# Performance work log

Hardware: AMD Instinct MI355X
Metric: run time of the kernel (lower is better)

The kernel has to match this reference:

```python
import jax, jax.numpy as jnp
import numpy as np

HEADS = 8
DIM_HEAD = 64
DIM = 512
SCALE = DIM ** -0.5  # NOTE: original scales by dim**-0.5, not dim_head**-0.5


def setup_inputs() -> dict:
    key = jax.random.key(0)
    k1, k2, k3 = jax.random.split(key, 3)
    b, n = 2, 4096
    x = jax.random.normal(k1, (b, n, DIM), dtype=jnp.float32)
    Wqkv = jax.random.normal(k2, (DIM, 3 * HEADS * DIM_HEAD), dtype=jnp.float32) * (DIM ** -0.5)
    Wout = jax.random.normal(k3, (HEADS * DIM_HEAD, DIM), dtype=jnp.float32) * ((HEADS * DIM_HEAD) ** -0.5)
    b_out = jnp.zeros((DIM,), dtype=jnp.float32)
    return {"x": x, "Wqkv": Wqkv, "Wout": Wout, "b_out": b_out}


def reference(x, Wqkv, Wout, b_out):
    b, n, _ = x.shape
    h, d = HEADS, DIM_HEAD
    qkv = x @ Wqkv  # [b, n, 3*h*d]
    q, k, v = jnp.split(qkv, 3, axis=-1)
    to_heads = lambda t: t.reshape(b, n, h, d).transpose(0, 2, 1, 3)  # [b,h,n,d]
    q, k, v = to_heads(q), to_heads(k), to_heads(v)
    half = n // 2
    q_s, q_t = q[:, :, :half], q[:, :, half:]
    k_t = k[:, :, half:]  # k_s is unused in the original module
    v_s, v_t = v[:, :, :half], v[:, :, half:]
    # temporal branch: q_t attends to k_t, reads v_t
    dots_t = jnp.einsum('bhid,bhjd->bhij', q_t, k_t) * SCALE
    # spatial branch: cross-term q_s attends to k_t, reads v_s
    dots_s = jnp.einsum('bhid,bhjd->bhij', q_s, k_t) * SCALE
    attn_s = jax.nn.softmax(dots_s, axis=-1)
    attn_t = jax.nn.softmax(dots_t, axis=-1)
    out_s = jnp.einsum('bhij,bhjd->bhid', attn_s, v_s)
    out_t = jnp.einsum('bhij,bhjd->bhid', attn_t, v_t)
    out = jnp.concatenate([out_s, out_t], axis=2)  # [b,h,n,d]
    out = out.transpose(0, 2, 1, 3).reshape(b, n, h * d)
    return out @ Wout + b_out
```

## Files before the change

### kernel.cpp

```cpp
#include <hip/hip_runtime.h>
#include <hip/hip_bf16.h>

typedef __bf16 bf16;
typedef _Float16 f16;
typedef __bf16 bf16x4 __attribute__((ext_vector_type(4)));
typedef __bf16 bf16x8 __attribute__((ext_vector_type(8)));
typedef _Float16 f16x4 __attribute__((ext_vector_type(4)));
typedef _Float16 f16x8 __attribute__((ext_vector_type(8)));
typedef float floatx4 __attribute__((ext_vector_type(4)));

static __device__ __forceinline__ floatx4 mfma_bf16(bf16x8 a, bf16x8 b, floatx4 c) {
  return __builtin_amdgcn_mfma_f32_16x16x32_bf16(a, b, c, 0, 0, 0);
}
static __device__ __forceinline__ floatx4 mfma_f16k32(f16x8 a, f16x8 b, floatx4 c) {
  return __builtin_amdgcn_mfma_f32_16x16x32_f16(a, b, c, 0, 0, 0);
}

static __device__ __forceinline__ void async16(void* lds, const void* gp) {
  __builtin_amdgcn_global_load_lds(
      (const __attribute__((address_space(1))) void*)gp,
      (__attribute__((address_space(3))) void*)lds, 16, 0, 0);
}

static __device__ __forceinline__ bf16x8 cvt8(float4 f0, float4 f1) {
  bf16x8 r;
  r[0] = (bf16)f0.x; r[1] = (bf16)f0.y; r[2] = (bf16)f0.z; r[3] = (bf16)f0.w;
  r[4] = (bf16)f1.x; r[5] = (bf16)f1.y; r[6] = (bf16)f1.z; r[7] = (bf16)f1.w;
  return r;
}

#define HEADS 8
#define DIMH 64
#define DIM 512
#define SEQ 4096
#define HALF 2048
#define BATCH 2
#define MROWS (BATCH * SEQ)
#define ELEMS ((size_t)MROWS * DIM)
#define NPARTS 4

#define C2F (0.044194173824159216f * 1.4426950408889634f)

__global__ __launch_bounds__(256)
void prep(const float* __restrict__ X, bf16* __restrict__ Xb,
          const float* __restrict__ wqkv, bf16* __restrict__ W1t,
          const float* __restrict__ wout, bf16* __restrict__ W2t) {
  __shared__ float tile[32][33];
  const int bid = blockIdx.x, t = threadIdx.x;
  if (bid < 2048) {
    size_t i = ((size_t)bid * 256 + t) * 8;
    float4 f0 = *reinterpret_cast<const float4*>(X + i);
    float4 f1 = *reinterpret_cast<const float4*>(X + i + 4);
    *reinterpret_cast<bf16x8*>(Xb + i) = cvt8(f0, f1);
    return;
  }
  const float* src; bf16* dst; int N, id;
  if (bid < 2816) { id = bid - 2048; src = wqkv; dst = W1t; N = 1536; }
  else            { id = bid - 2816; src = wout; dst = W2t; N = 512; }
  const int nb = N / 32;
  const int n0 = (id % nb) * 32, k0 = (id / nb) * 32;
  const int r = t >> 3, c4 = (t & 7) * 4;
  float4 v = *reinterpret_cast<const float4*>(src + (size_t)(k0 + r) * N + n0 + c4);
  tile[r][c4 + 0] = v.x; tile[r][c4 + 1] = v.y;
  tile[r][c4 + 2] = v.z; tile[r][c4 + 3] = v.w;
  __syncthreads();
  bf16x4 o;
#pragma unroll
  for (int i = 0; i < 4; ++i) o[i] = (bf16)tile[c4 + i][r];
  *reinterpret_cast<bf16x4*>(dst + (size_t)(n0 + r) * DIM + k0 + c4) = o;
}

__global__ __launch_bounds__(256)
void qkv_gemm(const bf16* __restrict__ Xb, const bf16* __restrict__ Wt,
              bf16* __restrict__ Qw, bf16* __restrict__ Kw, f16* __restrict__ Vt) {
  __shared__ __align__(16) char smem_raw[36864];

  const int m0 = blockIdx.x * 128, n0 = blockIdx.y * 128;
  const int t = threadIdx.x;
  const int wave = t >> 6, lane = t & 63, quad = lane >> 4, l16 = lane & 15;
  const int wr = wave >> 1, wc = wave & 1;

  f16 (*Ts)[72] = (f16(*)[72])(smem_raw + wave * 9216);

  floatx4 acc[4][4] = {};

  auto issue = [&](int buf, int k0) {
    bf16* Asf = (bf16*)(smem_raw + buf * 16384);
    bf16* Bsf = Asf + 4096;
#pragma unroll
    for (int it = 0; it < 2; ++it) {
      int g = it * 256 + t, row = g >> 2, c8 = (g & 3) * 8;
      async16(Asf + (size_t)g * 8, Xb + (size_t)(m0 + row) * DIM + k0 + c8);
      async16(Bsf + (size_t)g * 8, Wt + (size_t)(n0 + row) * DIM + k0 + c8);
    }
  };

  issue(0, 0);
  int buf = 0;
#pragma unroll 1
  for (int k0 = 0; k0 < DIM; k0 += 32) {
    __syncthreads();
    if (k0 + 32 < DIM) issue(buf ^ 1, k0 + 32);

    const bf16* Asf = (const bf16*)(smem_raw + buf * 16384);
    const bf16* Bsf = Asf + 4096;
    bf16x8 af[4], bfr[4];
#pragma unroll
    for (int mi = 0; mi < 4; ++mi)
      af[mi] = *reinterpret_cast<const bf16x8*>(
          Asf + (size_t)(wr * 64 + mi * 16 + l16) * 32 + quad * 8);
#pragma unroll
    for (int ni = 0; ni < 4; ++ni)
      bfr[ni] = *reinterpret_cast<const bf16x8*>(
          Bsf + (size_t)(wc * 64 + ni * 16 + l16) * 32 + quad * 8);
#pragma unroll
    for (int mi = 0; mi < 4; ++mi)
#pragma unroll
      for (int ni = 0; ni < 4; ++ni)
        acc[mi][ni] = mfma_bf16(af[mi], bfr[ni], acc[mi][ni]);
    buf ^= 1;
  }

  if (n0 < 1024) {
#pragma unroll
    for (int mi = 0; mi < 4; ++mi)
#pragma unroll
      for (int ni = 0; ni < 4; ++ni)
#pragma unroll
        for (int r = 0; r < 4; ++r) {
          int row = m0 + wr * 64 + mi * 16 + quad * 4 + r;
          int col = n0 + wc * 64 + ni * 16 + l16;
          int which = col >> 9, cc = col & 511;
          int head = cc >> 6, dim = cc & 63;
          int bb = row >> 12, nn = row & 4095;
          float val = acc[mi][ni][r];
          if (which == 0) val *= C2F;
          bf16* dst = which ? Kw : Qw;
          dst[(((size_t)(bb * HEADS + head)) * SEQ + nn) * DIMH + dim] = (bf16)val;
        }
  } else {
    __syncthreads();
    int head = (n0 + wc * 64 - 1024) >> 6;
#pragma unroll
    for (int mi = 0; mi < 4; ++mi)
#pragma unroll
      for (int ni = 0; ni < 4; ++ni) {
        f16x4 pv;
#pragma unroll
        for (int r = 0; r < 4; ++r) pv[r] = (f16)acc[mi][ni][r];
        *reinterpret_cast<f16x4*>(&Ts[ni * 16 + l16][mi * 16 + quad * 4]) = pv;
      }
    int bb = m0 >> 12, nnb = (m0 + wr * 64) & 4095;
    size_t base = ((size_t)(bb * HEADS + head)) * DIMH;
#pragma unroll
    for (int it = 0; it < 8; ++it) {
      int idx = lane + it * 64;
      int d = idx >> 3, ns = (idx & 7) * 8;
      *reinterpret_cast<f16x8*>(Vt + (base + d) * SEQ + nnb + ns) =
          *reinterpret_cast<const f16x8*>(&Ts[d][ns]);
    }
  }
}

__global__ __launch_bounds__(256)
void attn_kernel(const bf16* __restrict__ Q, const bf16* __restrict__ K,
                 const f16* __restrict__ Vt, f16* __restrict__ Opart,
                 float* __restrict__ Lpart) {
  const int qt = blockIdx.x;
  const int h = blockIdx.y;
  const int bb = blockIdx.z >> 2, part = blockIdx.z & 3;
  const int t = threadIdx.x;
  const int wave = t >> 6, lane = t & 63, quad = lane >> 4, l16 = lane & 15;

  __shared__ bf16 Ks[64][72];
  __shared__ f16 VsT[64][72];

  const size_t hb = ((size_t)(bb * HEADS + h)) * SEQ * DIMH;
  const int vhalf = (qt < 16) ? 0 : HALF;
  const int kstart = HALF + part * 512;
  const int vstart = vhalf + part * 512;
  const int q0 = qt * 128 + wave * 32;

  bf16x8 qa[2][2];
#pragma unroll
  for (int mt = 0; mt < 2; ++mt)
#pragma unroll
    for (int kc = 0; kc < 2; ++kc)
      qa[mt][kc] = *reinterpret_cast<const bf16x8*>(
          Q + hb + (size_t)(q0 + mt * 16 + l16) * DIMH + kc * 32 + quad * 8);

  floatx4 o_acc[2][4] = {};
  float l_acc[2] = {0.f, 0.f};

  int srow[2], sdst[2], g8s;
  {
    int r0 = t >> 3;  g8s = (t & 7) * 8;
#pragma unroll
    for (int it = 0; it < 2; ++it) {
      int row = r0 + it * 32;
      int g32 = row >> 5, w = row & 31, q = w >> 3, j = w & 7;
      int m = (j < 4) ? (4 * q + j) : (16 + 4 * q + (j - 4));
      srow[it] = row;
      sdst[it] = 32 * g32 + m;
    }
  }

  bf16x8 kreg[2];
  f16x8 vreg[2];
  auto loadc = [&](int kc0) {
#pragma unroll
    for (int it = 0; it < 2; ++it) {
      kreg[it] = *reinterpret_cast<const bf16x8*>(
          K + hb + (size_t)(kstart + kc0 + srow[it]) * DIMH + g8s);
      vreg[it] = *reinterpret_cast<const f16x8*>(
          Vt + hb + (size_t)srow[it] * SEQ + vstart + kc0 + g8s);
    }
  };

  loadc(0);
#pragma unroll 1
  for (int kc0 = 0; kc0 < 512; kc0 += 64) {
    __syncthreads();
#pragma unroll
    for (int it = 0; it < 2; ++it) {
      *reinterpret_cast<bf16x8*>(&Ks[sdst[it]][g8s]) = kreg[it];
      *reinterpret_cast<f16x8*>(&VsT[srow[it]][g8s]) = vreg[it];
    }
    __syncthreads();
    int nxt = kc0 + 64; if (nxt >= 512) nxt = 0;
    loadc(nxt);

#pragma unroll
    for (int g = 0; g < 2; ++g) {
      bf16x8 kaA0 = *reinterpret_cast<const bf16x8*>(&Ks[g * 32 + l16][quad * 8]);
      bf16x8 kaA1 = *reinterpret_cast<const bf16x8*>(&Ks[g * 32 + l16][32 + quad * 8]);
      bf16x8 kaB0 = *reinterpret_cast<const bf16x8*>(&Ks[g * 32 + 16 + l16][quad * 8]);
      bf16x8 kaB1 = *reinterpret_cast<const bf16x8*>(&Ks[g * 32 + 16 + l16][32 + quad * 8]);

      f16x8 pbm[2];
#pragma unroll
      for (int mt = 0; mt < 2; ++mt) {
        floatx4 stA = {0.f, 0.f, 0.f, 0.f}, stB = {0.f, 0.f, 0.f, 0.f};
        stA = mfma_bf16(kaA0, qa[mt][0], stA);
        stA = mfma_bf16(kaA1, qa[mt][1], stA);
        stB = mfma_bf16(kaB0, qa[mt][0], stB);
        stB = mfma_bf16(kaB1, qa[mt][1], stB);
        float ls = l_acc[mt];
        f16x8 pb;
#pragma unroll
        for (int r = 0; r < 4; ++r) {
          float pA = __builtin_amdgcn_exp2f(stA[r]);
          float pB = __builtin_amdgcn_exp2f(stB[r]);
          ls += pA + pB;
          pb[r] = (f16)pA;
          pb[4 + r] = (f16)pB;
        }
        l_acc[mt] = ls;
        pbm[mt] = pb;
      }

#pragma unroll
      for (int dsub = 0; dsub < 4; ++dsub) {
        f16x8 va = *reinterpret_cast<const f16x8*>(
            &VsT[dsub * 16 + l16][g * 32 + quad * 8]);
        o_acc[0][dsub] = mfma_f16k32(va, pbm[0], o_acc[0][dsub]);
        o_acc[1][dsub] = mfma_f16k32(va, pbm[1], o_acc[1][dsub]);
      }
    }
  }

  f16* Op = Opart + (size_t)part * ELEMS;
  float* Lp = Lpart + (size_t)part * MROWS * HEADS;
#pragma unroll
  for (int mt = 0; mt < 2; ++mt) {
    float v = l_acc[mt];
    v += __shfl_xor(v, 16);
    v += __shfl_xor(v, 32);
    int n = q0 + mt * 16 + l16;
    size_t rowidx = (size_t)(bb * SEQ + n);
    if (quad == 0) Lp[rowidx * HEADS + h] = v;
    size_t rowbase = rowidx * DIM + h * DIMH;
#pragma unroll
    for (int dsub = 0; dsub < 4; ++dsub) {
      f16x4 ov;
#pragma unroll
      for (int r = 0; r < 4; ++r) ov[r] = (f16)o_acc[mt][dsub][r];
      *reinterpret_cast<f16x4*>(Op + rowbase + dsub * 16 + quad * 4) = ov;
    }
  }
}

__global__ __launch_bounds__(256)
void out_gemm(const f16* __restrict__ Opart, const float* __restrict__ Lpart,
              const bf16* __restrict__ Wt, const float* __restrict__ bias,
              float* __restrict__ out) {
  __shared__ __align__(16) bf16 Asf[64 * 64];
  __shared__ __align__(16) bf16 Bsf[64 * 64];

  const int m0 = blockIdx.x * 64, n0 = blockIdx.y * 64;
  const int t = threadIdx.x;
  const int wave = t >> 6, lane = t & 63, quad = lane >> 4, l16 = lane & 15;
  const int m_off = (wave >> 1) * 32, n_off = (wave & 1) * 32;

  int srowi[2], sc8[2];
#pragma unroll
  for (int it = 0; it < 2; ++it) {
    int g = t + it * 256;
    srowi[it] = g >> 3; sc8[it] = (g & 7) * 8;
  }

  float linv[2][8];
#pragma unroll
  for (int it = 0; it < 2; ++it) {
    size_t ar = (size_t)(m0 + srowi[it]);
#pragma unroll
    for (int hh = 0; hh < 8; ++hh) {
      float s = 0.f;
#pragma unroll
      for (int p = 0; p < NPARTS; ++p)
        s += Lpart[(size_t)p * MROWS * HEADS + ar * HEADS + hh];
      linv[it][hh] = 1.0f / s;
    }
  }

  floatx4 acc[2][2] = {};

  f16x8 oreg[2][NPARTS];
  auto loadO = [&](int k0) {
#pragma unroll
    for (int it = 0; it < 2; ++it) {
      size_t abase = (size_t)(m0 + srowi[it]) * DIM + k0 + sc8[it];
#pragma unroll
      for (int p = 0; p < NPARTS; ++p)
        oreg[it][p] = *reinterpret_cast<const f16x8*>(Opart + (size_t)p * ELEMS + abase);
    }
  };

  loadO(0);
#pragma unroll 1
  for (int k0 = 0; k0 < DIM; k0 += 64) {
#pragma unroll
    for (int it = 0; it < 2; ++it) {
      int g = t + it * 256;
      async16(Bsf + (size_t)g * 8, Wt + (size_t)(n0 + srowi[it]) * DIM + k0 + sc8[it]);
      float inv = linv[it][(k0 + sc8[it]) >> 6];
      bf16x8 a;
#pragma unroll
      for (int j = 0; j < 8; ++j)
        a[j] = (bf16)(((float)oreg[it][0][j] + (float)oreg[it][1][j] +
                       (float)oreg[it][2][j] + (float)oreg[it][3][j]) * inv);
      *reinterpret_cast<bf16x8*>(Asf + (size_t)g * 8) = a;
    }
    __syncthreads();
    int nk = k0 + 64; if (nk >= DIM) nk = 0;
    loadO(nk);

#pragma unroll
    for (int kk = 0; kk < 2; ++kk) {
      bf16x8 a0 = *reinterpret_cast<const bf16x8*>(Asf + (size_t)(m_off + l16) * 64 + kk * 32 + quad * 8);
      bf16x8 a1 = *reinterpret_cast<const bf16x8*>(Asf + (size_t)(m_off + 16 + l16) * 64 + kk * 32 + quad * 8);
      bf16x8 b0 = *reinterpret_cast<const bf16x8*>(Bsf + (size_t)(n_off + l16) * 64 + kk * 32 + quad * 8);
      bf16x8 b1 = *reinterpret_cast<const bf16x8*>(Bsf + (size_t)(n_off + 16 + l16) * 64 + kk * 32 + quad * 8);
      acc[0][0] = mfma_bf16(a0, b0, acc[0][0]);
      acc[0][1] = mfma_bf16(a0, b1, acc[0][1]);
      acc[1][0] = mfma_bf16(a1, b0, acc[1][0]);
      acc[1][1] = mfma_bf16(a1, b1, acc[1][1]);
    }
    __syncthreads();
  }

#pragma unroll
  for (int mi = 0; mi < 2; ++mi)
#pragma unroll
    for (int ni = 0; ni < 2; ++ni)
#pragma unroll
      for (int r = 0; r < 4; ++r) {
        int row = m0 + m_off + mi * 16 + quad * 4 + r;
        int col = n0 + n_off + ni * 16 + l16;
        out[(size_t)row * DIM + col] = acc[mi][ni][r] + bias[col];
      }
}

extern "C" void kernel_launch(void* const* d_in, const int* in_sizes, int n_in,
                              void* d_out, int out_size, void* d_ws, size_t ws_size,
                              hipStream_t stream) {
  const float* x = (const float*)d_in[0];
  const float* wqkv = (const float*)d_in[1];
  const float* wout = (const float*)d_in[2];
  const float* bout = (const float*)d_in[3];
  float* out = (float*)d_out;

  char* ws = (char*)d_ws;
  f16* Opart = (f16*)ws;
  bf16* Xb = (bf16*)ws;
  bf16* Qw = (bf16*)(ws + ((size_t)32 << 20));
  bf16* Kw = Qw + ELEMS;
  f16* Vt = (f16*)(Kw + ELEMS);
  bf16* WtQKV = (bf16*)(Vt + ELEMS);
  bf16* WtOUT = WtQKV + (size_t)1536 * 512;
  float* Lpart = (float*)(WtOUT + (size_t)512 * 512);

  prep<<<3072, 256, 0, stream>>>(x, Xb, wqkv, WtQKV, wout, WtOUT);
  qkv_gemm<<<dim3(MROWS / 128, 1536 / 128), 256, 0, stream>>>(Xb, WtQKV, Qw, Kw, Vt);
  attn_kernel<<<dim3(SEQ / 128, HEADS, BATCH * NPARTS), 256, 0, stream>>>(Qw, Kw, Vt, Opart, Lpart);
  out_gemm<<<dim3(MROWS / 64, DIM / 64), 256, 0, stream>>>(Opart, Lpart, WtOUT, bout, out);
}
```

Measured before the change: 159.6 us.

## Use async LDS loads with XOR swizzle in attention and halve KV split

The attention kernel now stages K and V tiles into double-buffered LDS with direct global-to-LDS async loads using an XOR-swizzled layout, replacing the register-staged copy and its extra barrier. The KV sequence split drops from four parts to two, so each block processes 1024 keys, and the output GEMM sums fewer partials. The QKV and output GEMMs also adopt XOR swizzles to avoid LDS bank conflicts, and probability packing uses the packed round-toward-zero f16 conversion. Fewer parts means fewer blocks and less parallelism, but also less partial-output traffic.

```diff
diff --git a/kernel.cpp b/kernel.cpp
--- a/kernel.cpp
+++ b/kernel.cpp
@@ -5,6 +5,7 @@
 typedef _Float16 f16;
 typedef __bf16 bf16x4 __attribute__((ext_vector_type(4)));
 typedef __bf16 bf16x8 __attribute__((ext_vector_type(8)));
+typedef __fp16 fp16x2 __attribute__((ext_vector_type(2)));
 typedef _Float16 f16x4 __attribute__((ext_vector_type(4)));
 typedef _Float16 f16x8 __attribute__((ext_vector_type(8)));
 typedef float floatx4 __attribute__((ext_vector_type(4)));
@@ -37,7 +38,7 @@
 #define BATCH 2
 #define MROWS (BATCH * SEQ)
 #define ELEMS ((size_t)MROWS * DIM)
-#define NPARTS 4
+#define NPARTS 2
 
 #define C2F (0.044194173824159216f * 1.4426950408889634f)
 
@@ -84,14 +85,20 @@
 
   floatx4 acc[4][4] = {};
 
+  size_t srcOff[2];
+#pragma unroll
+  for (int it = 0; it < 2; ++it) {
+    int g = it * 256 + t, row = g >> 2, gs = (g & 3) ^ (row & 3);
+    srcOff[it] = (size_t)row * DIM + gs * 8;
+  }
   auto issue = [&](int buf, int k0) {
     bf16* Asf = (bf16*)(smem_raw + buf * 16384);
     bf16* Bsf = Asf + 4096;
 #pragma unroll
     for (int it = 0; it < 2; ++it) {
-      int g = it * 256 + t, row = g >> 2, c8 = (g & 3) * 8;
-      async16(Asf + (size_t)g * 8, Xb + (size_t)(m0 + row) * DIM + k0 + c8);
-      async16(Bsf + (size_t)g * 8, Wt + (size_t)(n0 + row) * DIM + k0 + c8);
+      int g = it * 256 + t;
+      async16(Asf + (size_t)g * 8, Xb + (size_t)m0 * DIM + k0 + srcOff[it]);
+      async16(Bsf + (size_t)g * 8, Wt + (size_t)n0 * DIM + k0 + srcOff[it]);
     }
   };
 
@@ -106,13 +113,15 @@
     const bf16* Bsf = Asf + 4096;
     bf16x8 af[4], bfr[4];
 #pragma unroll
-    for (int mi = 0; mi < 4; ++mi)
-      af[mi] = *reinterpret_cast<const bf16x8*>(
-          Asf + (size_t)(wr * 64 + mi * 16 + l16) * 32 + quad * 8);
-#pragma unroll
-    for (int ni = 0; ni < 4; ++ni)
-      bfr[ni] = *reinterpret_cast<const bf16x8*>(
-          Bsf + (size_t)(wc * 64 + ni * 16 + l16) * 32 + quad * 8);
+    for (int mi = 0; mi < 4; ++mi) {
+      int m = wr * 64 + mi * 16 + l16;
+      af[mi] = *reinterpret_cast<const bf16x8*>(Asf + (size_t)m * 32 + (quad ^ (m & 3)) * 8);
+    }
+#pragma unroll
+    for (int ni = 0; ni < 4; ++ni) {
+      int m = wc * 64 + ni * 16 + l16;
+      bfr[ni] = *reinterpret_cast<const bf16x8*>(Bsf + (size_t)m * 32 + (quad ^ (m & 3)) * 8);
+    }
 #pragma unroll
     for (int mi = 0; mi < 4; ++mi)
 #pragma unroll
@@ -168,17 +177,16 @@
                  float* __restrict__ Lpart) {
   const int qt = blockIdx.x;
   const int h = blockIdx.y;
-  const int bb = blockIdx.z >> 2, part = blockIdx.z & 3;
+  const int bb = blockIdx.z >> 1, part = blockIdx.z & 1;
   const int t = threadIdx.x;
   const int wave = t >> 6, lane = t & 63, quad = lane >> 4, l16 = lane & 15;
 
-  __shared__ bf16 Ks[64][72];
-  __shared__ f16 VsT[64][72];
+  __shared__ __align__(16) char smem[32768];
 
   const size_t hb = ((size_t)(bb * HEADS + h)) * SEQ * DIMH;
   const int vhalf = (qt < 16) ? 0 : HALF;
-  const int kstart = HALF + part * 512;
-  const int vstart = vhalf + part * 512;
+  const int kstart = HALF + part * 1024;
+  const int vstart = vhalf + part * 1024;
   const int q0 = qt * 128 + wave * 32;
 
   bf16x8 qa[2][2];
@@ -192,50 +200,43 @@
   floatx4 o_acc[2][4] = {};
   float l_acc[2] = {0.f, 0.f};
 
-  int srow[2], sdst[2], g8s;
-  {
-    int r0 = t >> 3;  g8s = (t & 7) * 8;
+  size_t kOff[2], vOff[2];
+#pragma unroll
+  for (int it = 0; it < 2; ++it) {
+    int G = it * 256 + t, row = G >> 3, gs = (G & 7) ^ (row & 7);
+    int m32 = row & 31, grp = row >> 5;
+    int w = 8 * ((m32 & 15) >> 2) + (m32 & 3) + ((m32 & 16) ? 4 : 0);
+    kOff[it] = (size_t)(grp * 32 + w) * DIMH + gs * 8;
+    vOff[it] = (size_t)row * SEQ + gs * 8;
+  }
+  auto issue = [&](int buf, int kc0) {
+    bf16* Kb = (bf16*)(smem + buf * 16384);
+    f16* Vb = (f16*)(smem + buf * 16384 + 8192);
 #pragma unroll
     for (int it = 0; it < 2; ++it) {
-      int row = r0 + it * 32;
-      int g32 = row >> 5, w = row & 31, q = w >> 3, j = w & 7;
-      int m = (j < 4) ? (4 * q + j) : (16 + 4 * q + (j - 4));
-      srow[it] = row;
-      sdst[it] = 32 * g32 + m;
-    }
-  }
-
-  bf16x8 kreg[2];
-  f16x8 vreg[2];
-  auto loadc = [&](int kc0) {
-#pragma unroll
-    for (int it = 0; it < 2; ++it) {
-      kreg[it] = *reinterpret_cast<const bf16x8*>(
-          K + hb + (size_t)(kstart + kc0 + srow[it]) * DIMH + g8s);
-      vreg[it] = *reinterpret_cast<const f16x8*>(
-          Vt + hb + (size_t)srow[it] * SEQ + vstart + kc0 + g8s);
+      int G = it * 256 + t;
+      async16(Kb + (size_t)G * 8, K + hb + (size_t)(kstart + kc0) * DIMH + kOff[it]);
+      async16(Vb + (size_t)G * 8, Vt + hb + (size_t)(vstart + kc0) + vOff[it]);
     }
   };
 
-  loadc(0);
+  issue(0, 0);
+  int buf = 0;
 #pragma unroll 1
-  for (int kc0 = 0; kc0 < 512; kc0 += 64) {
+  for (int kc0 = 0; kc0 < 1024; kc0 += 64) {
     __syncthreads();
-#pragma unroll
-    for (int it = 0; it < 2; ++it) {
-      *reinterpret_cast<bf16x8*>(&Ks[sdst[it]][g8s]) = kreg[it];
-      *reinterpret_cast<f16x8*>(&VsT[srow[it]][g8s]) = vreg[it];
-    }
-    __syncthreads();
-    int nxt = kc0 + 64; if (nxt >= 512) nxt = 0;
-    loadc(nxt);
-
-#pragma unroll
-    for (int g = 0; g < 2; ++g) {
-      bf16x8 kaA0 = *reinterpret_cast<const bf16x8*>(&Ks[g * 32 + l16][quad * 8]);
-      bf16x8 kaA1 = *reinterpret_cast<const bf16x8*>(&Ks[g * 32 + l16][32 + quad * 8]);
-      bf16x8 kaB0 = *reinterpret_cast<const bf16x8*>(&Ks[g * 32 + 16 + l16][quad * 8]);
-      bf16x8 kaB1 = *reinterpret_cast<const bf16x8*>(&Ks[g * 32 + 16 + l16][32 + quad * 8]);
+    if (kc0 + 64 < 1024) issue(buf ^ 1, kc0 + 64);
+
+    const bf16* Kb = (const bf16*)(smem + buf * 16384);
+    const f16* Vb = (const f16*)(smem + buf * 16384 + 8192);
+#pragma unroll
+    for (int gg = 0; gg < 2; ++gg) {
+      int mA = gg * 32 + l16, mB = mA + 16;
+      int s7 = l16 & 7;
+      bf16x8 kaA0 = *reinterpret_cast<const bf16x8*>(Kb + (size_t)mA * 64 + (quad ^ s7) * 8);
+      bf16x8 kaA1 = *reinterpret_cast<const bf16x8*>(Kb + (size_t)mA * 64 + ((4 + quad) ^ s7) * 8);
+      bf16x8 kaB0 = *reinterpret_cast<const bf16x8*>(Kb + (size_t)mB * 64 + (quad ^ s7) * 8);
+      bf16x8 kaB1 = *reinterpret_cast<const bf16x8*>(Kb + (size_t)mB * 64 + ((4 + quad) ^ s7) * 8);
 
       f16x8 pbm[2];
 #pragma unroll
@@ -245,28 +246,33 @@
         stA = mfma_bf16(kaA1, qa[mt][1], stA);
         stB = mfma_bf16(kaB0, qa[mt][0], stB);
         stB = mfma_bf16(kaB1, qa[mt][1], stB);
+        float pA[4], pB[4];
         float ls = l_acc[mt];
-        f16x8 pb;
 #pragma unroll
         for (int r = 0; r < 4; ++r) {
-          float pA = __builtin_amdgcn_exp2f(stA[r]);
-          float pB = __builtin_amdgcn_exp2f(stB[r]);
-          ls += pA + pB;
-          pb[r] = (f16)pA;
-          pb[4 + r] = (f16)pB;
+          pA[r] = __builtin_amdgcn_exp2f(stA[r]);
+          pB[r] = __builtin_amdgcn_exp2f(stB[r]);
+          ls += pA[r] + pB[r];
         }
         l_acc[mt] = ls;
-        pbm[mt] = pb;
+        union { f16x8 v8; fp16x2 v2[4]; } u;
+        u.v2[0] = __builtin_amdgcn_cvt_pkrtz(pA[0], pA[1]);
+        u.v2[1] = __builtin_amdgcn_cvt_pkrtz(pA[2], pA[3]);
+        u.v2[2] = __builtin_amdgcn_cvt_pkrtz(pB[0], pB[1]);
+        u.v2[3] = __builtin_amdgcn_cvt_pkrtz(pB[2], pB[3]);
+        pbm[mt] = u.v8;
       }
 
 #pragma unroll
       for (int dsub = 0; dsub < 4; ++dsub) {
+        int d = dsub * 16 + l16;
         f16x8 va = *reinterpret_cast<const f16x8*>(
-            &VsT[dsub * 16 + l16][g * 32 + quad * 8]);
+            Vb + (size_t)d * 64 + ((gg * 4 + quad) ^ (d & 7)) * 8);
         o_acc[0][dsub] = mfma_f16k32(va, pbm[0], o_acc[0][dsub]);
         o_acc[1][dsub] = mfma_f16k32(va, pbm[1], o_acc[1][dsub]);
       }
     }
+    buf ^= 1;
   }
 
   f16* Op = Opart + (size_t)part * ELEMS;
@@ -305,8 +311,9 @@
   int srowi[2], sc8[2];
 #pragma unroll
   for (int it = 0; it < 2; ++it) {
-    int g = t + it * 256;
-    srowi[it] = g >> 3; sc8[it] = (g & 7) * 8;
+    int g = t + it * 256, row = g >> 3;
+    srowi[it] = row;
+    sc8[it] = ((g & 7) ^ (row & 7)) * 8;
   }
 
   float linv[2][8];
@@ -343,12 +350,11 @@
     for (int it = 0; it < 2; ++it) {
       int g = t + it * 256;
       async16(Bsf + (size_t)g * 8, Wt + (size_t)(n0 + srowi[it]) * DIM + k0 + sc8[it]);
-      float inv = linv[it][(k0 + sc8[it]) >> 6];
+      float inv = linv[it][k0 >> 6];
       bf16x8 a;
 #pragma unroll
       for (int j = 0; j < 8; ++j)
-        a[j] = (bf16)(((float)oreg[it][0][j] + (float)oreg[it][1][j] +
-                       (float)oreg[it][2][j] + (float)oreg[it][3][j]) * inv);
+        a[j] = (bf16)(((float)oreg[it][0][j] + (float)oreg[it][1][j]) * inv);
       *reinterpret_cast<bf16x8*>(Asf + (size_t)g * 8) = a;
     }
     __syncthreads();
@@ -357,10 +363,13 @@
 
 #pragma unroll
     for (int kk = 0; kk < 2; ++kk) {
-      bf16x8 a0 = *reinterpret_cast<const bf16x8*>(Asf + (size_t)(m_off + l16) * 64 + kk * 32 + quad * 8);
-      bf16x8 a1 = *reinterpret_cast<const bf16x8*>(Asf + (size_t)(m_off + 16 + l16) * 64 + kk * 32 + quad * 8);
-      bf16x8 b0 = *reinterpret_cast<const bf16x8*>(Bsf + (size_t)(n_off + l16) * 64 + kk * 32 + quad * 8);
-      bf16x8 b1 = *reinterpret_cast<const bf16x8*>(Bsf + (size_t)(n_off + 16 + l16) * 64 + kk * 32 + quad * 8);
+      int mA0 = m_off + l16, mA1 = m_off + 16 + l16;
+      int nB0 = n_off + l16, nB1 = n_off + 16 + l16;
+      int q = kk * 4 + quad;
+      bf16x8 a0 = *reinterpret_cast<const bf16x8*>(Asf + (size_t)mA0 * 64 + (q ^ (mA0 & 7)) * 8);
+      bf16x8 a1 = *reinterpret_cast<const bf16x8*>(Asf + (size_t)mA1 * 64 + (q ^ (mA1 & 7)) * 8);
+      bf16x8 b0 = *reinterpret_cast<const bf16x8*>(Bsf + (size_t)nB0 * 64 + (q ^ (nB0 & 7)) * 8);
+      bf16x8 b1 = *reinterpret_cast<const bf16x8*>(Bsf + (size_t)nB1 * 64 + (q ^ (nB1 & 7)) * 8);
       acc[0][0] = mfma_bf16(a0, b0, acc[0][0]);
       acc[0][1] = mfma_bf16(a0, b1, acc[0][1]);
       acc[1][0] = mfma_bf16(a1, b0, acc[1][0]);
@@ -393,7 +402,7 @@
   char* ws = (char*)d_ws;
   f16* Opart = (f16*)ws;
   bf16* Xb = (bf16*)ws;
-  bf16* Qw = (bf16*)(ws + ((size_t)32 << 20));
+  bf16* Qw = (bf16*)(ws + ((size_t)16 << 20));
   bf16* Kw = Qw + ELEMS;
   f16* Vt = (f16*)(Kw + ELEMS);
   bf16* WtQKV = (bf16*)(Vt + ELEMS);
```

Result: slower. 164.6 us (+3.1%).
